# Kernel optimization log

Measured on AMD Instinct MI355X. Metric: run time of the kernel, lower is better.

Reference implementation:

```python
import jax, jax.numpy as jnp
import numpy as np

B, S, D, H = 4, 2048, 1024, 16
HD = D // H  # head_dim = 64


def setup_inputs() -> dict:
    key = jax.random.key(0)
    ks = jax.random.split(key, 5)
    scale = 1.0 / np.sqrt(D)
    return {
        "x": jax.random.normal(ks[0], (B, S, D), dtype=jnp.float32),
        "Wq": jax.random.normal(ks[1], (D, D), dtype=jnp.float32) * scale,
        "Wk": jax.random.normal(ks[2], (D, D), dtype=jnp.float32) * scale,
        "Wv": jax.random.normal(ks[3], (D, D), dtype=jnp.float32) * scale,
        "Wo": jax.random.normal(ks[4], (D, D), dtype=jnp.float32) * scale,
        "bo": jnp.zeros((D,), dtype=jnp.float32),
    }


def reference(x, Wq, Wk, Wv, Wo, bo):
    b, n, d_in = x.shape
    # projections: [b, n, d_out] -> [b, h, n, hd]
    def heads(t):
        return t.reshape(b, n, H, HD).transpose(0, 2, 1, 3)
    q = heads(x @ Wq)
    k = heads(x @ Wk)
    v = heads(x @ Wv)
    # attention scores [b, h, n, n], causal mask, scaled softmax
    scores = jnp.einsum('bhqd,bhkd->bhqk', q, k)
    causal = jnp.tril(jnp.ones((n, n), dtype=bool))  # True = keep
    scores = jnp.where(causal, scores, -jnp.inf)
    weights = jax.nn.softmax(scores / np.sqrt(HD), axis=-1)
    # context: [b, h, n, hd] -> [b, n, d_out]
    ctx = jnp.einsum('bhqk,bhkd->bhqd', weights, v)
    ctx = ctx.transpose(0, 2, 1, 3).reshape(b, n, D)
    return ctx @ Wo + bo
```

## Files before the change

kernel.cpp:

```cpp
#include <hip/hip_runtime.h>

#define B_ 4
#define S_ 2048
#define D_ 1024
#define H_ 16
#define HD_ 64

typedef __bf16 bf16x8 __attribute__((ext_vector_type(8)));
typedef float f32x4 __attribute__((ext_vector_type(4)));
typedef float f32x16 __attribute__((ext_vector_type(16)));
typedef unsigned short u16;
typedef unsigned short u16x8 __attribute__((ext_vector_type(8)));

__device__ __forceinline__ u16 f2b(float f) {
  unsigned u = __builtin_bit_cast(unsigned, f);
  return (u16)((u + 0x7FFFu + ((u >> 16) & 1u)) >> 16);
}

__device__ __forceinline__ void gll16(const void* g, void* l) {
  __builtin_amdgcn_global_load_lds(
      (const __attribute__((address_space(1))) void*)g,
      (__attribute__((address_space(3))) void*)l, 16, 0, 0);
}

__device__ __forceinline__ f32x4 mfma16(bf16x8 a, bf16x8 b, f32x4 c) {
  return __builtin_amdgcn_mfma_f32_16x16x32_bf16(a, b, c, 0, 0, 0);
}
__device__ __forceinline__ f32x16 mfma32(bf16x8 a, bf16x8 b, f32x16 c) {
  return __builtin_amdgcn_mfma_f32_32x32x16_bf16(a, b, c, 0, 0, 0);
}

__device__ __forceinline__ unsigned cvtpk(float lo, float hi) {
  unsigned r;
  asm("v_cvt_pk_bf16_f32 %0, %1, %2" : "=v"(r) : "v"(lo), "v"(hi));
  return r;
}
__device__ __forceinline__ void plswap(unsigned& a, unsigned& b) {
  asm("v_permlane32_swap_b32 %0, %1" : "+v"(a), "+v"(b));
}
__device__ __forceinline__ bf16x8 mk8(unsigned a, unsigned b, unsigned c, unsigned d) {
  union { unsigned u[4]; bf16x8 v; } x;
  x.u[0] = a; x.u[1] = b; x.u[2] = c; x.u[3] = d;
  return x.v;
}

__global__ __launch_bounds__(256) void k_pre(
    const float* __restrict__ x, u16* __restrict__ xb,
    const float* __restrict__ Wq, const float* __restrict__ Wk,
    const float* __restrict__ Wv, const float* __restrict__ Wo,
    u16* __restrict__ wqkvt, u16* __restrict__ wot) {
  const int t = threadIdx.x;
  if (blockIdx.x < 8192) {
    int i = blockIdx.x * 256 + t;
    float4 f = reinterpret_cast<const float4*>(x)[i];
    ushort4 o;
    o.x = f2b(f.x); o.y = f2b(f.y); o.z = f2b(f.z); o.w = f2b(f.w);
    reinterpret_cast<ushort4*>(xb)[i] = o;
    return;
  }
  __shared__ float tile[32][33];
  const int id = blockIdx.x - 8192;
  const int z = id >> 10;
  const float* W;
  u16* Wt;
  if (z == 0)      { W = Wq; Wt = wqkvt; }
  else if (z == 1) { W = Wk; Wt = wqkvt + (size_t)D_ * D_; }
  else if (z == 2) { W = Wv; Wt = wqkvt + (size_t)2 * D_ * D_; }
  else             { W = Wo; Wt = wot; }
  const int bx = (id & 31) * 32, by = ((id >> 5) & 31) * 32;
  const int tx = t & 31, ty = t >> 5;
  #pragma unroll
  for (int i = ty; i < 32; i += 8)
    tile[i][tx] = W[(size_t)(by + i) * D_ + bx + tx];
  __syncthreads();
  #pragma unroll
  for (int i = ty; i < 32; i += 8)
    Wt[(size_t)(bx + i) * D_ + by + tx] = f2b(tile[tx][i]);
}

__global__ __launch_bounds__(512, 2) void k_gemm_qk(
    const u16* __restrict__ A, const u16* __restrict__ Bt,
    u16* __restrict__ q, u16* __restrict__ kk) {
  constexpr int K = D_;
  constexpr int NT = K / 64;
  __shared__ __align__(16) u16 lA[2 * 256 * 64];
  __shared__ __align__(16) u16 lB[2 * 256 * 64];
  const int cpx = 32;
  const int id = blockIdx.x;
  const int swz = (id & 7) * cpx + (id >> 3);
  const int bx = swz & 7, by = swz >> 3;
  const int m0 = by * 256, n0 = bx * 256;
  const int t = threadIdx.x, lane = t & 63, w = t >> 6;
  const int wr = w >> 2, wc = w & 3;
  const int lr = lane & 15, lg = lane >> 4;
  const int l7 = lr & 7;
  const int wrlr = wr * 16 + lr, wclr = wc * 16 + lr;
  const int srow = t >> 3;
  const int sch = (t & 7) ^ (srow & 7);
  const u16* gAs = A + (size_t)(m0 + srow) * K + sch * 8;
  const u16* gBs = Bt + (size_t)(n0 + srow) * K + sch * 8;

  f32x4 acc[8][4] = {};
  bf16x8 Af[4][2], Bf0[2][2], Bf1[2][2];

  auto stageN = [&](int n) {
    if (n >= 4 * NT) return;
    const int kt2 = n >> 2, idx = n & 3;
    const int mat = idx & 1;
    const int h = (idx == 1 || idx == 2);
    const int bo = (kt2 & 1) * 16384;
    const u16* g = (mat ? gBs : gAs) + (size_t)(h * 128) * K + kt2 * 64;
    u16* l = (mat ? lB : lA) + bo + h * 8192 + t * 8;
    gll16(g, l);
    gll16(g + (size_t)64 * K, l + 4096);
  };

#define LOAD_A(qa_)                                                           \
  _Pragma("unroll") for (int il = 0; il < 4; ++il)                            \
  _Pragma("unroll") for (int ks = 0; ks < 2; ++ks)                            \
    Af[il][ks] = *(const bf16x8*)&lA[bufo + ((qa_)*128 + il * 32 + wrlr) * 64 +\
                                     (((ks * 4 + lg) ^ l7) * 8)];
#define LOAD_B(dst_, qb_)                                                     \
  _Pragma("unroll") for (int jl = 0; jl < 2; ++jl)                            \
  _Pragma("unroll") for (int ks = 0; ks < 2; ++ks)                            \
    dst_[jl][ks] = *(const bf16x8*)&lB[bufo + ((qb_)*128 + jl * 64 + wclr) * 64 +\
                                       (((ks * 4 + lg) ^ l7) * 8)];
#define MF(qa_, qb_, bf_)                                                     \
  __builtin_amdgcn_s_setprio(1);                                              \
  _Pragma("unroll") for (int il = 0; il < 4; ++il)                            \
  _Pragma("unroll") for (int jl = 0; jl < 2; ++jl)                            \
  _Pragma("unroll") for (int ks = 0; ks < 2; ++ks)                            \
    acc[(qa_)*4 + il][(qb_)*2 + jl] =                                         \
        mfma16(Af[il][ks], bf_[jl][ks], acc[(qa_)*4 + il][(qb_)*2 + jl]);     \
  __builtin_amdgcn_s_setprio(0);
#define BAR asm volatile("s_barrier" ::: "memory");
#define LGKM0 asm volatile("s_waitcnt lgkmcnt(0)" ::: "memory");

  stageN(0); stageN(1); stageN(3);
  stageN(2);
  stageN(4); stageN(5); stageN(7);

  for (int kt = 0; kt < NT; ++kt) {
    const int bufo = (kt & 1) * 16384;
    stageN(4 * (kt + 1) + 2);
    if (kt < NT - 1) {
      asm volatile("s_waitcnt vmcnt(8)" ::: "memory");
    } else {
      asm volatile("s_waitcnt vmcnt(0)" ::: "memory");
    }
    BAR
    LOAD_A(0) LOAD_B(Bf0, 0) LOAD_B(Bf1, 1)
    LGKM0
    MF(0, 0, Bf0) MF(0, 1, Bf1)
    BAR
    stageN(4 * (kt + 2) + 0);
    stageN(4 * (kt + 2) + 1);
    stageN(4 * (kt + 2) + 3);
    LOAD_A(1)
    LGKM0
    MF(1, 0, Bf0) MF(1, 1, Bf1)
    BAR
  }
#undef LOAD_A
#undef LOAD_B
#undef MF

  const int nclass = bx >> 2;
  const int b2 = m0 >> 11;
  const int s0b = m0 & 2047;
  const int h0 = (n0 & 1023) >> 6;
  u16* dst = nclass == 0 ? q : kk;
  const float sc = nclass == 0 ? 0.1803368801111f : 1.0f;
  #pragma unroll
  for (int i = 0; i < 8; ++i)
    #pragma unroll
    for (int j = 0; j < 4; ++j) {
      const size_t bh = (size_t)b2 * H_ + h0 + j;
      #pragma unroll
      for (int r = 0; r < 4; ++r) {
        int mloc = i * 32 + wr * 16 + lg * 4 + r;
        dst[(bh * S_ + s0b + mloc) * HD_ + wc * 16 + lr] =
            f2b(acc[i][j][r] * sc);
      }
    }
}

__global__ __launch_bounds__(512, 1) void k_gemm_v(
    const u16* __restrict__ A, const u16* __restrict__ Bt,
    u16* __restrict__ v) {
  constexpr int K = D_;
  constexpr int NT = K / 64;
  __shared__ __align__(16) u16 lA[2 * 128 * 64];
  __shared__ __align__(16) u16 lB[2 * 256 * 64];
  const int cpx = 32;
  const int id = blockIdx.x;
  const int swz = (id & 7) * cpx + (id >> 3);
  const int bx = swz & 3, by = swz >> 2;
  const int m0 = by * 128, n0 = bx * 256;
  const int t = threadIdx.x, lane = t & 63, w = t >> 6;
  const int wr = w >> 2, wc = w & 3;
  const int lr = lane & 15, lg = lane >> 4;
  const int l7 = lr & 7;
  const int wrlr = wr * 16 + lr, wclr = wc * 16 + lr;
  const int srow = t >> 3;
  const int sch = (t & 7) ^ (srow & 7);
  const u16* gAs = A + (size_t)(m0 + srow) * K + sch * 8;
  const u16* gBs = Bt + (size_t)(n0 + srow) * K + sch * 8;

  f32x4 acc[4][4] = {};
  bf16x8 Af[2][2], Bf0[2][2], Bf1[2][2];

  auto stageN = [&](int n) {
    if (n >= 4 * NT) return;
    const int kt2 = n >> 2, idx = n & 3;
    const int koff = kt2 * 64;
    if (idx == 0) {
      gll16(gAs + koff, &lA[(kt2 & 1) * 8192 + t * 8]);
    } else if (idx == 2) {
      gll16(gAs + (size_t)64 * K + koff, &lA[(kt2 & 1) * 8192 + 4096 + t * 8]);
    } else if (idx == 1) {
      const u16* g = gBs + (size_t)128 * K + koff;
      u16* l = &lB[(kt2 & 1) * 16384 + 8192 + t * 8];
      gll16(g, l);
      gll16(g + (size_t)64 * K, l + 4096);
    } else {
      const u16* g = gBs + koff;
      u16* l = &lB[(kt2 & 1) * 16384 + t * 8];
      gll16(g, l);
      gll16(g + (size_t)64 * K, l + 4096);
    }
  };

#define LOAD_A(qa_)                                                           \
  _Pragma("unroll") for (int il = 0; il < 2; ++il)                            \
  _Pragma("unroll") for (int ks = 0; ks < 2; ++ks)                            \
    Af[il][ks] = *(const bf16x8*)&lA[bufoA + ((qa_)*64 + il * 32 + wrlr) * 64 +\
                                     (((ks * 4 + lg) ^ l7) * 8)];
#define LOAD_B(dst_, qb_)                                                     \
  _Pragma("unroll") for (int jl = 0; jl < 2; ++jl)                            \
  _Pragma("unroll") for (int ks = 0; ks < 2; ++ks)                            \
    dst_[jl][ks] = *(const bf16x8*)&lB[bufoB + ((qb_)*128 + jl * 64 + wclr) * 64 +\
                                       (((ks * 4 + lg) ^ l7) * 8)];
#define MF(qa_, qb_, bf_)                                                     \
  __builtin_amdgcn_s_setprio(1);                                              \
  _Pragma("unroll") for (int il = 0; il < 2; ++il)                            \
  _Pragma("unroll") for (int jl = 0; jl < 2; ++jl)                            \
  _Pragma("unroll") for (int ks = 0; ks < 2; ++ks)                            \
    acc[(qa_)*2 + il][(qb_)*2 + jl] =                                         \
        mfma16(Af[il][ks], bf_[jl][ks], acc[(qa_)*2 + il][(qb_)*2 + jl]);     \
  __builtin_amdgcn_s_setprio(0);

  stageN(0); stageN(1); stageN(3);
  stageN(2);
  stageN(4); stageN(5); stageN(7);

  for (int kt = 0; kt < NT; ++kt) {
    const int bufoA = (kt & 1) * 8192;
    const int bufoB = (kt & 1) * 16384;
    stageN(4 * (kt + 1) + 2);
    if (kt < NT - 1) {
      asm volatile("s_waitcnt vmcnt(6)" ::: "memory");
    } else {
      asm volatile("s_waitcnt vmcnt(0)" ::: "memory");
    }
    BAR
    LOAD_A(0) LOAD_B(Bf0, 0) LOAD_B(Bf1, 1)
    LGKM0
    MF(0, 0, Bf0) MF(0, 1, Bf1)
    BAR
    stageN(4 * (kt + 2) + 0);
    stageN(4 * (kt + 2) + 1);
    stageN(4 * (kt + 2) + 3);
    LOAD_A(1)
    LGKM0
    MF(1, 0, Bf0) MF(1, 1, Bf1)
    BAR
  }
#undef LOAD_A
#undef LOAD_B
#undef MF
#undef BAR
#undef LGKM0

  const int b2 = m0 >> 11;
  const int s0b = m0 & 2047;
  const int h0 = n0 >> 6;
  u16* vb = (u16*)lA;
  const int row = t >> 3, col0 = (t & 7) * 16;
  #pragma unroll
  for (int nj = 0; nj < 4; ++nj) {
    __syncthreads();
    #pragma unroll
    for (int mi = 0; mi < 4; ++mi)
      #pragma unroll
      for (int r = 0; r < 4; ++r)
        vb[(wc * 16 + lr) * 136 + mi * 32 + wr * 16 + lg * 4 + r] =
            f2b(acc[mi][nj][r]);
    __syncthreads();
    u16* gv = v + ((size_t)(b2 * H_ + h0 + nj) * HD_ + row) * S_ + s0b + col0;
    *(u16x8*)(gv) = *(const u16x8*)&vb[row * 136 + col0];
    *(u16x8*)(gv + 8) = *(const u16x8*)&vb[row * 136 + col0 + 8];
  }
}

__global__ __launch_bounds__(512, 1) void k_gemm_proj2(
    const u16* __restrict__ A, const u16* __restrict__ Bt,
    const float* __restrict__ bias, float* __restrict__ out) {
  constexpr int K = D_;
  constexpr int NT = K / 64;
  __shared__ __align__(16) u16 lA[2 * 128 * 64];
  __shared__ __align__(16) u16 lB[2 * 256 * 64];
  const int cpx = 32;
  const int id = blockIdx.x;
  const int swz = (id & 7) * cpx + (id >> 3);
  const int bx = swz & 3, by = swz >> 2;
  const int m0 = by * 128, n0 = bx * 256;
  const int t = threadIdx.x, lane = t & 63, w = t >> 6;
  const int wr = w >> 2, wc = w & 3;
  const int lr = lane & 15, lg = lane >> 4;
  const int l7 = lr & 7;
  const int wrlr = wr * 16 + lr, wclr = wc * 16 + lr;
  const int srow = t >> 3;
  const int sch = (t & 7) ^ (srow & 7);
  const u16* gAs = A + (size_t)(m0 + srow) * K + sch * 8;
  const u16* gBs = Bt + (size_t)(n0 + srow) * K + sch * 8;

  f32x4 acc[4][4] = {};
  bf16x8 Af[2][2], Bf0[2][2], Bf1[2][2];

  auto stageN = [&](int n) {
    if (n >= 4 * NT) return;
    const int kt2 = n >> 2, idx = n & 3;
    const int koff = kt2 * 64;
    if (idx == 0) {
      gll16(gAs + koff, &lA[(kt2 & 1) * 8192 + t * 8]);
    } else if (idx == 2) {
      gll16(gAs + (size_t)64 * K + koff, &lA[(kt2 & 1) * 8192 + 4096 + t * 8]);
    } else if (idx == 1) {
      const u16* g = gBs + (size_t)128 * K + koff;
      u16* l = &lB[(kt2 & 1) * 16384 + 8192 + t * 8];
      gll16(g, l);
      gll16(g + (size_t)64 * K, l + 4096);
    } else {
      const u16* g = gBs + koff;
      u16* l = &lB[(kt2 & 1) * 16384 + t * 8];
      gll16(g, l);
      gll16(g + (size_t)64 * K, l + 4096);
    }
  };

#define LOAD_A(qa_)                                                           \
  _Pragma("unroll") for (int il = 0; il < 2; ++il)                            \
  _Pragma("unroll") for (int ks = 0; ks < 2; ++ks)                            \
    Af[il][ks] = *(const bf16x8*)&lA[bufoA + ((qa_)*64 + il * 32 + wrlr) * 64 +\
                                     (((ks * 4 + lg) ^ l7) * 8)];
#define LOAD_B(dst_, qb_)                                                     \
  _Pragma("unroll") for (int jl = 0; jl < 2; ++jl)                            \
  _Pragma("unroll") for (int ks = 0; ks < 2; ++ks)                            \
    dst_[jl][ks] = *(const bf16x8*)&lB[bufoB + ((qb_)*128 + jl * 64 + wclr) * 64 +\
                                       (((ks * 4 + lg) ^ l7) * 8)];
#define MF(qa_, qb_, bf_)                                                     \
  __builtin_amdgcn_s_setprio(1);                                              \
  _Pragma("unroll") for (int il = 0; il < 2; ++il)                            \
  _Pragma("unroll") for (int jl = 0; jl < 2; ++jl)                            \
  _Pragma("unroll") for (int ks = 0; ks < 2; ++ks)                            \
    acc[(qa_)*2 + il][(qb_)*2 + jl] =                                         \
        mfma16(Af[il][ks], bf_[jl][ks], acc[(qa_)*2 + il][(qb_)*2 + jl]);     \
  __builtin_amdgcn_s_setprio(0);
#define BAR asm volatile("s_barrier" ::: "memory");
#define LGKM0 asm volatile("s_waitcnt lgkmcnt(0)" ::: "memory");

  stageN(0); stageN(1); stageN(3);
  stageN(2);
  stageN(4); stageN(5); stageN(7);

  for (int kt = 0; kt < NT; ++kt) {
    const int bufoA = (kt & 1) * 8192;
    const int bufoB = (kt & 1) * 16384;
    stageN(4 * (kt + 1) + 2);
    if (kt < NT - 1) {
      asm volatile("s_waitcnt vmcnt(6)" ::: "memory");
    } else {
      asm volatile("s_waitcnt vmcnt(0)" ::: "memory");
    }
    BAR
    LOAD_A(0) LOAD_B(Bf0, 0) LOAD_B(Bf1, 1)
    LGKM0
    MF(0, 0, Bf0) MF(0, 1, Bf1)
    BAR
    stageN(4 * (kt + 2) + 0);
    stageN(4 * (kt + 2) + 1);
    stageN(4 * (kt + 2) + 3);
    LOAD_A(1)
    LGKM0
    MF(1, 0, Bf0) MF(1, 1, Bf1)
    BAR
  }
#undef LOAD_A
#undef LOAD_B
#undef MF
#undef BAR
#undef LGKM0

  float bv[4];
  int nn[4];
  #pragma unroll
  for (int nj = 0; nj < 4; ++nj) {
    nn[nj] = n0 + (nj >> 1) * 128 + (nj & 1) * 64 + wc * 16 + lr;
    bv[nj] = bias[nn[nj]];
  }
  #pragma unroll
  for (int mi = 0; mi < 4; ++mi) {
    #pragma unroll
    for (int nj = 0; nj < 4; ++nj) {
      #pragma unroll
      for (int r = 0; r < 4; ++r) {
        int m = m0 + (mi >> 1) * 64 + (mi & 1) * 32 + wr * 16 + lg * 4 + r;
        out[(size_t)m * D_ + nn[nj]] = acc[mi][nj][r] + bv[nj];
      }
    }
  }
}

__global__ __launch_bounds__(256, 2) void k_attn(
    const u16* __restrict__ Qg, const u16* __restrict__ Kg,
    const u16* __restrict__ Vtg, u16* __restrict__ ctx) {
  __shared__ __align__(16) u16 Ks[2][64 * 64];
  __shared__ __align__(16) u16 Vs[2][64 * 64];
  const int ja = blockIdx.y, jb = 15 - ja, bh = blockIdx.x;
  const int t = threadIdx.x, l = t & 63, wq = t >> 6;
  const int lo5 = l & 31, hi = l >> 5, sw = l & 7;
  const size_t base = (size_t)bh * S_ * HD_;
  const int srow = t >> 3, sch = (t & 7) ^ (srow & 7);

  const int qw0A = ja * 128 + wq * 32, qw0B = jb * 128 + wq * 32;
  const int dktA = qw0A >> 6, dktB = qw0B >> 6;

  bf16x8 qA[4], qB[4];
  {
    const u16* qp = Qg + base + (size_t)(qw0A + lo5) * HD_ + hi * 8;
    #pragma unroll
    for (int di = 0; di < 4; ++di) qA[di] = *(const bf16x8*)(qp + di * 16);
    qp = Qg + base + (size_t)(qw0B + lo5) * HD_ + hi * 8;
    #pragma unroll
    for (int di = 0; di < 4; ++di) qB[di] = *(const bf16x8*)(qp + di * 16);
  }
  float lsA = 0.f, lsB = 0.f;
  f32x16 oA0 = {}, oA1 = {}, oB0 = {}, oB1 = {};

  auto stage = [&](int buf, int kb) {
    gll16(Kg + base + (size_t)(kb + srow) * HD_ + sch * 8, &Ks[buf][t * 8]);
    gll16(Kg + base + (size_t)(kb + 32 + srow) * HD_ + sch * 8, &Ks[buf][2048 + t * 8]);
    gll16(Vtg + base + (size_t)srow * S_ + kb + sch * 8, &Vs[buf][t * 8]);
    gll16(Vtg + base + (size_t)(32 + srow) * S_ + kb + sch * 8, &Vs[buf][2048 + t * 8]);
  };

  auto attend = [&](int buf, int kt, int qw0, int dkt, const bf16x8 (&qf)[4],
                    float& l_r, f32x16& o0, f32x16& o1) {
    const u16* KB = &Ks[buf][0];
    const u16* VB = &Vs[buf][0];
    f32x16 s0 = {}, s1 = {};
    #pragma unroll
    for (int di = 0; di < 4; ++di)
      s0 = mfma32(*(const bf16x8*)&KB[lo5 * 64 + (((di * 2 + hi) ^ sw) * 8)],
                  qf[di], s0);
    #pragma unroll
    for (int di = 0; di < 4; ++di)
      s1 = mfma32(*(const bf16x8*)&KB[(32 + lo5) * 64 + (((di * 2 + hi) ^ sw) * 8)],
                  qf[di], s1);
    if (kt == dkt) {
      int qrel = qw0 + lo5 - kt * 64;
      #pragma unroll
      for (int r = 0; r < 16; ++r) {
        int k0 = (r & 3) + 8 * (r >> 2) + 4 * hi;
        if (k0 > qrel) s0[r] = -1e30f;
        if (k0 + 32 > qrel) s1[r] = -1e30f;
      }
    }
    #pragma unroll
    for (int r = 0; r < 16; ++r) s0[r] = __builtin_amdgcn_exp2f(s0[r] - 8.f);
    #pragma unroll
    for (int r = 0; r < 16; ++r) s1[r] = __builtin_amdgcn_exp2f(s1[r] - 8.f);
    float sm[16];
    #pragma unroll
    for (int i = 0; i < 16; ++i) sm[i] = s0[i] + s1[i];
    #pragma unroll
    for (int st = 8; st >= 1; st >>= 1)
      #pragma unroll
      for (int i = 0; i < st; ++i) sm[i] += sm[i + st];
    l_r += sm[0] + __shfl_xor(sm[0], 32);
    unsigned a0 = cvtpk(s0[0], s0[1]), b0 = cvtpk(s0[4], s0[5]); plswap(a0, b0);
    unsigned a1 = cvtpk(s0[2], s0[3]), b1 = cvtpk(s0[6], s0[7]); plswap(a1, b1);
    unsigned a2 = cvtpk(s0[8], s0[9]), b2 = cvtpk(s0[12], s0[13]); plswap(a2, b2);
    unsigned a3 = cvtpk(s0[10], s0[11]), b3 = cvtpk(s0[14], s0[15]); plswap(a3, b3);
    bf16x8 p0 = mk8(a0, a1, b0, b1), p1 = mk8(a2, a3, b2, b3);
    a0 = cvtpk(s1[0], s1[1]); b0 = cvtpk(s1[4], s1[5]); plswap(a0, b0);
    a1 = cvtpk(s1[2], s1[3]); b1 = cvtpk(s1[6], s1[7]); plswap(a1, b1);
    a2 = cvtpk(s1[8], s1[9]); b2 = cvtpk(s1[12], s1[13]); plswap(a2, b2);
    a3 = cvtpk(s1[10], s1[11]); b3 = cvtpk(s1[14], s1[15]); plswap(a3, b3);
    bf16x8 p2 = mk8(a0, a1, b0, b1), p3 = mk8(a2, a3, b2, b3);
    o0 = mfma32(*(const bf16x8*)&VB[lo5 * 64 + (((0 + hi) ^ sw) * 8)], p0, o0);
    o0 = mfma32(*(const bf16x8*)&VB[lo5 * 64 + (((2 + hi) ^ sw) * 8)], p1, o0);
    o0 = mfma32(*(const bf16x8*)&VB[lo5 * 64 + (((4 + hi) ^ sw) * 8)], p2, o0);
    o0 = mfma32(*(const bf16x8*)&VB[lo5 * 64 + (((6 + hi) ^ sw) * 8)], p3, o0);
    o1 = mfma32(*(const bf16x8*)&VB[(32 + lo5) * 64 + (((0 + hi) ^ sw) * 8)], p0, o1);
    o1 = mfma32(*(const bf16x8*)&VB[(32 + lo5) * 64 + (((2 + hi) ^ sw) * 8)], p1, o1);
    o1 = mfma32(*(const bf16x8*)&VB[(32 + lo5) * 64 + (((4 + hi) ^ sw) * 8)], p2, o1);
    o1 = mfma32(*(const bf16x8*)&VB[(32 + lo5) * 64 + (((6 + hi) ^ sw) * 8)], p3, o1);
  };

  const int nt = 2 * jb + 2;
  stage(0, 0);
  __syncthreads();
  int cur = 0;
  for (int kt = 0; kt < nt; ++kt) {
    if (kt + 1 < nt) stage(cur ^ 1, (kt + 1) * 64);
    if (kt <= dktA) attend(cur, kt, qw0A, dktA, qA, lsA, oA0, oA1);
    if (kt <= dktB) attend(cur, kt, qw0B, dktB, qB, lsB, oB0, oB1);
    __syncthreads();
    cur ^= 1;
  }

  const int b = bh >> 4, h = bh & 15;
  {
    float inv = 1.f / lsA;
    u16* cp = ctx + ((size_t)b * S_ + qw0A + lo5) * D_ + h * 64 + hi * 4;
    #pragma unroll
    for (int rg = 0; rg < 4; ++rg) {
      ushort4 o4;
      o4.x = f2b(oA0[rg * 4 + 0] * inv); o4.y = f2b(oA0[rg * 4 + 1] * inv);
      o4.z = f2b(oA0[rg * 4 + 2] * inv); o4.w = f2b(oA0[rg * 4 + 3] * inv);
      *(ushort4*)(cp + rg * 8) = o4;
      o4.x = f2b(oA1[rg * 4 + 0] * inv); o4.y = f2b(oA1[rg * 4 + 1] * inv);
      o4.z = f2b(oA1[rg * 4 + 2] * inv); o4.w = f2b(oA1[rg * 4 + 3] * inv);
      *(ushort4*)(cp + 32 + rg * 8) = o4;
    }
  }
  {
    float inv = 1.f / lsB;
    u16* cp = ctx + ((size_t)b * S_ + qw0B + lo5) * D_ + h * 64 + hi * 4;
    #pragma unroll
    for (int rg = 0; rg < 4; ++rg) {
      ushort4 o4;
      o4.x = f2b(oB0[rg * 4 + 0] * inv); o4.y = f2b(oB0[rg * 4 + 1] * inv);
      o4.z = f2b(oB0[rg * 4 + 2] * inv); o4.w = f2b(oB0[rg * 4 + 3] * inv);
      *(ushort4*)(cp + rg * 8) = o4;
      o4.x = f2b(oB1[rg * 4 + 0] * inv); o4.y = f2b(oB1[rg * 4 + 1] * inv);
      o4.z = f2b(oB1[rg * 4 + 2] * inv); o4.w = f2b(oB1[rg * 4 + 3] * inv);
      *(ushort4*)(cp + 32 + rg * 8) = o4;
    }
  }
}

extern "C" void kernel_launch(void* const* d_in, const int* in_sizes, int n_in,
                              void* d_out, int out_size, void* d_ws, size_t ws_size,
                              hipStream_t stream) {
  const float* x  = (const float*)d_in[0];
  const float* Wq = (const float*)d_in[1];
  const float* Wk = (const float*)d_in[2];
  const float* Wv = (const float*)d_in[3];
  const float* Wo = (const float*)d_in[4];
  const float* bo = (const float*)d_in[5];
  float* out = (float*)d_out;
  (void)in_sizes; (void)n_in; (void)out_size; (void)ws_size;

  char* p = (char*)d_ws;
  const size_t NTOK = (size_t)B_ * S_;
  u16* xb    = (u16*)p; p += NTOK * D_ * 2;
  u16* wqkvt = (u16*)p; p += (size_t)3 * D_ * D_ * 2;
  u16* wot   = (u16*)p; p += (size_t)D_ * D_ * 2;
  u16* Qg    = (u16*)p; p += NTOK * D_ * 2;
  u16* Kg    = (u16*)p; p += NTOK * D_ * 2;
  u16* Vtg   = (u16*)p; p += NTOK * D_ * 2;
  u16* ctx   = (u16*)p; p += NTOK * D_ * 2;

  k_pre<<<dim3(8192 + 4096), dim3(256), 0, stream>>>(x, xb, Wq, Wk, Wv, Wo,
                                                     wqkvt, wot);
  k_gemm_qk<<<dim3(256), dim3(512), 0, stream>>>(xb, wqkvt, Qg, Kg);
  k_gemm_v<<<dim3(256), dim3(512), 0, stream>>>(
      xb, wqkvt + (size_t)2 * D_ * D_, Vtg);
  k_attn<<<dim3(B_ * H_, 8), dim3(256), 0, stream>>>(Qg, Kg, Vtg, ctx);
  k_gemm_proj2<<<dim3(256), dim3(512), 0, stream>>>(ctx, wot, bo, out);
}
```

Before: 164.3 us.

## Process two K/V tiles per barrier in causal attention loop

The attention kernel now stages two 64-key K/V tiles per pipeline step, double-buffered, and attends both before each barrier. This halves the number of __syncthreads and load-issue rounds per key range and gives each prefetch more compute to hide behind. The cost is doubled LDS use (64KB per block), which may limit the two-blocks-per-CU occupancy target. The always-run first attend for the B query block relies on nt being even and kp never exceeding dktB.

```diff
diff --git a/kernel.cpp b/kernel.cpp
--- a/kernel.cpp
+++ b/kernel.cpp
@@ -425,8 +425,8 @@
 __global__ __launch_bounds__(256, 2) void k_attn(
     const u16* __restrict__ Qg, const u16* __restrict__ Kg,
     const u16* __restrict__ Vtg, u16* __restrict__ ctx) {
-  __shared__ __align__(16) u16 Ks[2][64 * 64];
-  __shared__ __align__(16) u16 Vs[2][64 * 64];
+  __shared__ __align__(16) u16 Ks[2][2][64 * 64];
+  __shared__ __align__(16) u16 Vs[2][2][64 * 64];
   const int ja = blockIdx.y, jb = 15 - ja, bh = blockIdx.x;
   const int t = threadIdx.x, l = t & 63, wq = t >> 6;
   const int lo5 = l & 31, hi = l >> 5, sw = l & 7;
@@ -448,17 +448,19 @@
   float lsA = 0.f, lsB = 0.f;
   f32x16 oA0 = {}, oA1 = {}, oB0 = {}, oB1 = {};
 
-  auto stage = [&](int buf, int kb) {
-    gll16(Kg + base + (size_t)(kb + srow) * HD_ + sch * 8, &Ks[buf][t * 8]);
-    gll16(Kg + base + (size_t)(kb + 32 + srow) * HD_ + sch * 8, &Ks[buf][2048 + t * 8]);
-    gll16(Vtg + base + (size_t)srow * S_ + kb + sch * 8, &Vs[buf][t * 8]);
-    gll16(Vtg + base + (size_t)(32 + srow) * S_ + kb + sch * 8, &Vs[buf][2048 + t * 8]);
+  auto stage = [&](int buf, int sub, int kb) {
+    gll16(Kg + base + (size_t)(kb + srow) * HD_ + sch * 8, &Ks[buf][sub][t * 8]);
+    gll16(Kg + base + (size_t)(kb + 32 + srow) * HD_ + sch * 8,
+          &Ks[buf][sub][2048 + t * 8]);
+    gll16(Vtg + base + (size_t)srow * S_ + kb + sch * 8, &Vs[buf][sub][t * 8]);
+    gll16(Vtg + base + (size_t)(32 + srow) * S_ + kb + sch * 8,
+          &Vs[buf][sub][2048 + t * 8]);
   };
 
-  auto attend = [&](int buf, int kt, int qw0, int dkt, const bf16x8 (&qf)[4],
-                    float& l_r, f32x16& o0, f32x16& o1) {
-    const u16* KB = &Ks[buf][0];
-    const u16* VB = &Vs[buf][0];
+  auto attend = [&](int buf, int sub, int kt, int qw0, int dkt,
+                    const bf16x8 (&qf)[4], float& l_r, f32x16& o0, f32x16& o1) {
+    const u16* KB = &Ks[buf][sub][0];
+    const u16* VB = &Vs[buf][sub][0];
     f32x16 s0 = {}, s1 = {};
     #pragma unroll
     for (int di = 0; di < 4; ++di)
@@ -510,13 +512,19 @@
   };
 
   const int nt = 2 * jb + 2;
-  stage(0, 0);
+  stage(0, 0, 0);
+  stage(0, 1, 64);
   __syncthreads();
   int cur = 0;
-  for (int kt = 0; kt < nt; ++kt) {
-    if (kt + 1 < nt) stage(cur ^ 1, (kt + 1) * 64);
-    if (kt <= dktA) attend(cur, kt, qw0A, dktA, qA, lsA, oA0, oA1);
-    if (kt <= dktB) attend(cur, kt, qw0B, dktB, qB, lsB, oB0, oB1);
+  for (int kp = 0; kp < nt; kp += 2) {
+    if (kp + 2 < nt) {
+      stage(cur ^ 1, 0, (kp + 2) * 64);
+      stage(cur ^ 1, 1, (kp + 3) * 64);
+    }
+    if (kp <= dktA) attend(cur, 0, kp, qw0A, dktA, qA, lsA, oA0, oA1);
+    attend(cur, 0, kp, qw0B, dktB, qB, lsB, oB0, oB1);
+    if (kp + 1 <= dktA) attend(cur, 1, kp + 1, qw0A, dktA, qA, lsA, oA0, oA1);
+    if (kp + 1 <= dktB) attend(cur, 1, kp + 1, qw0B, dktB, qB, lsB, oB0, oB1);
     __syncthreads();
     cur ^= 1;
   }
```

After: 163.2 us. No clear change (-0.7%).

## Split paired causal query tiles into separate blocks, heaviest first

Applied to the files above, without the earlier changes.

The attention kernel previously paired a light and a heavy 128-row query tile in each block so every block did balanced work over a shared K/V stream. Now each block handles one query tile, the grid doubles to 16 tiles per head, blocks are ordered heaviest-first, and launch bounds ask for 4 blocks per CU. This gives more parallelism and lower register pressure, but loses the K/V tile reuse between the two paired tiles, so K/V global/LDS traffic roughly doubles and per-block work becomes unbalanced.

```diff
diff --git a/kernel.cpp b/kernel.cpp
--- a/kernel.cpp
+++ b/kernel.cpp
@@ -422,31 +422,28 @@
   }
 }
 
-__global__ __launch_bounds__(256, 2) void k_attn(
+__global__ __launch_bounds__(256, 4) void k_attn(
     const u16* __restrict__ Qg, const u16* __restrict__ Kg,
     const u16* __restrict__ Vtg, u16* __restrict__ ctx) {
   __shared__ __align__(16) u16 Ks[2][64 * 64];
   __shared__ __align__(16) u16 Vs[2][64 * 64];
-  const int ja = blockIdx.y, jb = 15 - ja, bh = blockIdx.x;
+  const int ja = 15 - blockIdx.y, bh = blockIdx.x;
   const int t = threadIdx.x, l = t & 63, wq = t >> 6;
   const int lo5 = l & 31, hi = l >> 5, sw = l & 7;
   const size_t base = (size_t)bh * S_ * HD_;
   const int srow = t >> 3, sch = (t & 7) ^ (srow & 7);
 
-  const int qw0A = ja * 128 + wq * 32, qw0B = jb * 128 + wq * 32;
-  const int dktA = qw0A >> 6, dktB = qw0B >> 6;
-
-  bf16x8 qA[4], qB[4];
+  const int qw0 = ja * 128 + wq * 32;
+  const int dkt = qw0 >> 6;
+
+  bf16x8 qf[4];
   {
-    const u16* qp = Qg + base + (size_t)(qw0A + lo5) * HD_ + hi * 8;
-    #pragma unroll
-    for (int di = 0; di < 4; ++di) qA[di] = *(const bf16x8*)(qp + di * 16);
-    qp = Qg + base + (size_t)(qw0B + lo5) * HD_ + hi * 8;
-    #pragma unroll
-    for (int di = 0; di < 4; ++di) qB[di] = *(const bf16x8*)(qp + di * 16);
-  }
-  float lsA = 0.f, lsB = 0.f;
-  f32x16 oA0 = {}, oA1 = {}, oB0 = {}, oB1 = {};
+    const u16* qp = Qg + base + (size_t)(qw0 + lo5) * HD_ + hi * 8;
+    #pragma unroll
+    for (int di = 0; di < 4; ++di) qf[di] = *(const bf16x8*)(qp + di * 16);
+  }
+  float ls = 0.f;
+  f32x16 o0 = {}, o1 = {};
 
   auto stage = [&](int buf, int kb) {
     gll16(Kg + base + (size_t)(kb + srow) * HD_ + sch * 8, &Ks[buf][t * 8]);
@@ -455,8 +452,7 @@
     gll16(Vtg + base + (size_t)(32 + srow) * S_ + kb + sch * 8, &Vs[buf][2048 + t * 8]);
   };
 
-  auto attend = [&](int buf, int kt, int qw0, int dkt, const bf16x8 (&qf)[4],
-                    float& l_r, f32x16& o0, f32x16& o1) {
+  auto attend = [&](int buf, int kt) {
     const u16* KB = &Ks[buf][0];
     const u16* VB = &Vs[buf][0];
     f32x16 s0 = {}, s1 = {};
@@ -488,7 +484,7 @@
     for (int st = 8; st >= 1; st >>= 1)
       #pragma unroll
       for (int i = 0; i < st; ++i) sm[i] += sm[i + st];
-    l_r += sm[0] + __shfl_xor(sm[0], 32);
+    ls += sm[0] + __shfl_xor(sm[0], 32);
     unsigned a0 = cvtpk(s0[0], s0[1]), b0 = cvtpk(s0[4], s0[5]); plswap(a0, b0);
     unsigned a1 = cvtpk(s0[2], s0[3]), b1 = cvtpk(s0[6], s0[7]); plswap(a1, b1);
     unsigned a2 = cvtpk(s0[8], s0[9]), b2 = cvtpk(s0[12], s0[13]); plswap(a2, b2);
@@ -509,46 +505,29 @@
     o1 = mfma32(*(const bf16x8*)&VB[(32 + lo5) * 64 + (((6 + hi) ^ sw) * 8)], p3, o1);
   };
 
-  const int nt = 2 * jb + 2;
+  const int nt = 2 * ja + 2;
   stage(0, 0);
   __syncthreads();
   int cur = 0;
   for (int kt = 0; kt < nt; ++kt) {
     if (kt + 1 < nt) stage(cur ^ 1, (kt + 1) * 64);
-    if (kt <= dktA) attend(cur, kt, qw0A, dktA, qA, lsA, oA0, oA1);
-    if (kt <= dktB) attend(cur, kt, qw0B, dktB, qB, lsB, oB0, oB1);
+    if (kt <= dkt) attend(cur, kt);
     __syncthreads();
     cur ^= 1;
   }
 
   const int b = bh >> 4, h = bh & 15;
-  {
-    float inv = 1.f / lsA;
-    u16* cp = ctx + ((size_t)b * S_ + qw0A + lo5) * D_ + h * 64 + hi * 4;
-    #pragma unroll
-    for (int rg = 0; rg < 4; ++rg) {
-      ushort4 o4;
-      o4.x = f2b(oA0[rg * 4 + 0] * inv); o4.y = f2b(oA0[rg * 4 + 1] * inv);
-      o4.z = f2b(oA0[rg * 4 + 2] * inv); o4.w = f2b(oA0[rg * 4 + 3] * inv);
-      *(ushort4*)(cp + rg * 8) = o4;
-      o4.x = f2b(oA1[rg * 4 + 0] * inv); o4.y = f2b(oA1[rg * 4 + 1] * inv);
-      o4.z = f2b(oA1[rg * 4 + 2] * inv); o4.w = f2b(oA1[rg * 4 + 3] * inv);
-      *(ushort4*)(cp + 32 + rg * 8) = o4;
-    }
-  }
-  {
-    float inv = 1.f / lsB;
-    u16* cp = ctx + ((size_t)b * S_ + qw0B + lo5) * D_ + h * 64 + hi * 4;
-    #pragma unroll
-    for (int rg = 0; rg < 4; ++rg) {
-      ushort4 o4;
-      o4.x = f2b(oB0[rg * 4 + 0] * inv); o4.y = f2b(oB0[rg * 4 + 1] * inv);
-      o4.z = f2b(oB0[rg * 4 + 2] * inv); o4.w = f2b(oB0[rg * 4 + 3] * inv);
-      *(ushort4*)(cp + rg * 8) = o4;
-      o4.x = f2b(oB1[rg * 4 + 0] * inv); o4.y = f2b(oB1[rg * 4 + 1] * inv);
-      o4.z = f2b(oB1[rg * 4 + 2] * inv); o4.w = f2b(oB1[rg * 4 + 3] * inv);
-      *(ushort4*)(cp + 32 + rg * 8) = o4;
-    }
+  float inv = 1.f / ls;
+  u16* cp = ctx + ((size_t)b * S_ + qw0 + lo5) * D_ + h * 64 + hi * 4;
+  #pragma unroll
+  for (int rg = 0; rg < 4; ++rg) {
+    ushort4 o4;
+    o4.x = f2b(o0[rg * 4 + 0] * inv); o4.y = f2b(o0[rg * 4 + 1] * inv);
+    o4.z = f2b(o0[rg * 4 + 2] * inv); o4.w = f2b(o0[rg * 4 + 3] * inv);
+    *(ushort4*)(cp + rg * 8) = o4;
+    o4.x = f2b(o1[rg * 4 + 0] * inv); o4.y = f2b(o1[rg * 4 + 1] * inv);
+    o4.z = f2b(o1[rg * 4 + 2] * inv); o4.w = f2b(o1[rg * 4 + 3] * inv);
+    *(ushort4*)(cp + 32 + rg * 8) = o4;
   }
 }
 
@@ -579,6 +558,6 @@
   k_gemm_qk<<<dim3(256), dim3(512), 0, stream>>>(xb, wqkvt, Qg, Kg);
   k_gemm_v<<<dim3(256), dim3(512), 0, stream>>>(
       xb, wqkvt + (size_t)2 * D_ * D_, Vtg);
-  k_attn<<<dim3(B_ * H_, 8), dim3(256), 0, stream>>>(Qg, Kg, Vtg, ctx);
+  k_attn<<<dim3(B_ * H_, 16), dim3(256), 0, stream>>>(Qg, Kg, Vtg, ctx);
   k_gemm_proj2<<<dim3(256), dim3(512), 0, stream>>>(ctx, wot, bo, out);
 }
```

Result: slower. 180.6 us (+9.9%).
